# Performance work log

Hardware: AMD Instinct MI355X
Metric: run time of the kernel (lower is better)

Reference implementation:

```python
import jax, jax.numpy as jnp
import numpy as np
import math
from jax import lax

EPS = 1e-4
# scale is clamped to [-2.5, 2.5] => std = 2**scale <= 2**2.5, filtersize = ceil(3*std+0.5) <= 18
FMAX = 18


def _conv3(x, w, b):
    y = lax.conv_general_dilated(x, w, (1, 1), [(1, 1), (1, 1)],
                                 dimension_numbers=('NCHW', 'OIHW', 'NCHW'))
    return y + b[None, :, None, None]


def _conv1(x, w, b):
    return jnp.einsum('oc,bchw->bohw', w[:, :, 0, 0], x) + b[None, :, None, None]


def _basis_filters(scale):
    # per-sample Gaussian basis (g, dg/dx, dg/dy) on a fixed 37x37 grid,
    # exactly zero-masked beyond the data-dependent filtersize before normalization
    std = 2.0 ** scale
    f = jnp.ceil(3.0 * std + 0.5)
    x = jnp.arange(-FMAX, FMAX + 1, dtype=jnp.float32)
    m1 = (jnp.abs(x) <= f).astype(jnp.float32)
    X, Y = jnp.meshgrid(x, x, indexing='ij')  # torch.meshgrid default 'ij'
    m = m1[:, None] * m1[None, :]
    gx = jnp.exp(-(X / std) ** 2 / 2)
    gy = jnp.exp(-(Y / std) ** 2 / 2)
    g = gx * gy * m
    g = g / jnp.sum(g)
    c = std ** 3 * 2 * math.pi
    dgdx = (-X / c) * gx * gy * m
    dgdx = dgdx / jnp.sum(jnp.abs(dgdx))
    dgdy = (-Y / c) * gy * gx * m
    dgdy = dgdy / jnp.sum(jnp.abs(dgdy))
    return jnp.stack([g, dgdx, dgdy])  # [3, 37, 37]


def _gauss_conv(img, w):
    # img [3,H,W] = (E, El, Ell) planes; w [3,k,k] = (g, dgdx, dgdy)
    # treat the 3 planes as a batch of single-channel images -> [3,3,H,W]
    return lax.conv_general_dilated(img[:, None], w[:, None], (1, 1),
                                    [(FMAX, FMAX), (FMAX, FMAX)],
                                    dimension_numbers=('NCHW', 'OIHW', 'NCHW'))


def setup_inputs() -> dict:
    key = jax.random.key(0)
    B, H, W = 8, 384, 384
    nmid, base = 64, 16
    ks = iter(jax.random.split(key, 32))

    def rn(shape, s=0.1):
        return jax.random.normal(next(ks), shape, dtype=jnp.float32) * s

    x = jax.random.uniform(next(ks), (B, 3, H, W), dtype=jnp.float32)
    gcm = jnp.array([[0.06, 0.63, 0.27], [0.3, 0.04, -0.35], [0.34, -0.6, 0.17]],
                    dtype=jnp.float32)
    return {
        'x': x, 'gcm': gcm,
        'convH_w': rn((base, 1, 1, 1)), 'convH_b': rn((base,), 0.01),
        'convS_w': rn((base, 1, 1, 1)), 'convS_b': rn((base,), 0.01),
        'convRGB_w': rn((base, 3, 1, 1)), 'convRGB_b': rn((base,), 0.01),
        'convWw_w': rn((base, 1, 1, 1)), 'convWw_b': rn((base,), 0.01),
        'convadj_w': rn((nmid, 4 * base, 1, 1)), 'convadj_b': rn((nmid,), 0.01),
        'c0_w': rn((16, 3, 3, 3)), 'c0_b': rn((16,), 0.01),
        'c1_w': rn((16, 16, 3, 3)), 'c1_b': rn((16,), 0.01),
        'c2_w': rn((1, 16, 3, 3)), 'c2_b': rn((1,), 0.01),
        'wp0_w': rn((16, 3, 3, 3)), 'wp0_b': rn((16,), 0.01),
        'wp1_w': rn((16, 16, 3, 3)), 'wp1_b': rn((16,), 0.01),
        'wp2_w': rn((4, 16, 1, 1)), 'wp2_b': rn((4,), 0.01),
    }


def reference(x, gcm, convH_w, convH_b, convS_w, convS_b, convRGB_w, convRGB_b,
              convWw_w, convWw_b, convadj_w, convadj_b,
              c0_w, c0_b, c1_w, c1_b, c2_w, c2_b,
              wp0_w, wp0_b, wp1_w, wp1_b, wp2_w, wp2_b):
    # --- RGB ordering (torch.no_grad + scatter_add == sum of one-hots) ---
    xi = lax.stop_gradient(x)
    oh = lambda i: jax.nn.one_hot(i, 3, axis=1, dtype=x.dtype)
    mx, mn = jnp.argmax(xi, axis=1), jnp.argmin(xi, axis=1)
    mx_ = 2 - jnp.argmax(xi[:, ::-1], axis=1)
    mn_ = 2 - jnp.argmin(xi[:, ::-1], axis=1)
    RGB_order = 0.5 * (oh(mx) + oh(mx_)) - 0.5 * (oh(mn) + oh(mn_))
    # --- per-sample scale from small convnet ---
    s = jax.nn.silu(_conv3(x, c0_w, c0_b))
    s = jax.nn.silu(_conv3(s, c1_w, c1_b))
    s = _conv3(s, c2_w, c2_b)
    scale = jnp.clip(jnp.mean(s, axis=(1, 2, 3)), -2.5, 2.5)  # [B]
    # --- Gaussian color model transform ---
    xg = jnp.einsum('ij,bjhw->bihw', gcm, x)  # [B,3,H,W]
    # --- per-sample scale-dependent Gaussian-derivative convolution ---
    filters = jax.vmap(_basis_filters)(scale)       # [B,3,37,37]
    outs = jax.vmap(_gauss_conv)(xg, filters)       # [B,3,3,H,W]: plane x basis
    E, Ex, Ey = outs[:, 0, 0:1], outs[:, 0, 1:2], outs[:, 0, 2:3]
    El, Ell = outs[:, 1, 0:1], outs[:, 2, 0:1]
    Hc = jnp.arctan(El / (Ell + EPS))
    Sc = jnp.log((El ** 2 + Ell ** 2) / (E ** 2 + EPS) + EPS)
    Ww = jnp.arctan((Ex / (E + EPS)) ** 2 + (Ey / (E + EPS)) ** 2)
    # --- fusion weight predictor (on gcm-transformed image, softmax over 4) ---
    w = jax.nn.relu(_conv3(xg, wp0_w, wp0_b))
    w = jax.nn.relu(_conv3(w, wp1_w, wp1_b))
    weights = jax.nn.softmax(_conv1(w, wp2_w, wp2_b), axis=1)  # [B,4,H,W]
    H_fea_w = _conv1(Hc, convH_w, convH_b) * weights[:, 0:1]
    S_fea_w = _conv1(Sc, convS_w, convS_b) * weights[:, 1:2]
    RGB_fea_w = _conv1(RGB_order, convRGB_w, convRGB_b) * weights[:, 2:3]
    Ww_fea_w = jnp.zeros_like(H_fea_w)  # ablation == 'no_Ww' (default)
    del Ww  # computed for fidelity; zeroed by ablation
    feats = jnp.concatenate([H_fea_w, S_fea_w, RGB_fea_w, Ww_fea_w], axis=1)
    return _conv1(feats, convadj_w, convadj_b)  # [B, n_fea_middle, H, W]
```

## Files before the change

### kernel.cpp

```cpp
#include <hip/hip_runtime.h>

#define HH 384
#define WW 384
#define HWS (HH*WW)
#define NB 8
#define EPSV 1e-4f

typedef unsigned int u32;
typedef unsigned short u16;
typedef __attribute__((ext_vector_type(8))) short bf16x8;
typedef __attribute__((ext_vector_type(4))) float f32x4;

__device__ inline float bf2f(u16 h) { return __uint_as_float(((u32)h) << 16); }
__device__ inline u16 f2bf(float f) {
  u32 u = __float_as_uint(f);
  return (u16)((u + 0x7fffu + ((u >> 16) & 1u)) >> 16);
}
__device__ inline float fc4(const float4& v, int i) {
  return i == 0 ? v.x : i == 1 ? v.y : i == 2 ? v.z : v.w;
}

__global__ void k_prep(const float* __restrict__ adj_w,
                       const float* __restrict__ convH_w, const float* __restrict__ convH_b,
                       const float* __restrict__ convS_w, const float* __restrict__ convS_b,
                       const float* __restrict__ convRGB_w, const float* __restrict__ convRGB_b,
                       const float* __restrict__ gcm,
                       const float* __restrict__ c0_w, const float* __restrict__ wp0_w,
                       const float* __restrict__ c1_w, const float* __restrict__ wp1_w,
                       float* __restrict__ coef, float* __restrict__ c0t,
                       float* __restrict__ w0g, u32* __restrict__ wpk1,
                       u32* __restrict__ wpk2, float* __restrict__ sums) {
  int t = threadIdx.x;
  for (int i = t; i < NB * 16 * 9; i += 256) sums[i] = 0.f;
  for (int i = t; i < 432; i += 256) {
    int o = i & 15, rem = i >> 4;
    int c = rem / 9, k9 = rem - c * 9;
    c0t[i] = c0_w[(o * 3 + c) * 9 + k9];
    float s = 0.f;
    for (int j = 0; j < 3; j++) s += wp0_w[(o * 3 + j) * 9 + k9] * gcm[j * 3 + c];
    w0g[i] = s;
  }
  for (int i = t; i < 1280; i += 256) {
    int p = i >> 8;
    int rem = i & 255;
    int l = rem >> 2, wq = rem & 3;
    int tp = 2 * p + (l >> 5);
    int oc = l & 15;
    int ic0 = ((l >> 4) & 1) * 8 + wq * 2;
    u32 v1 = 0, v2 = 0;
    if (tp < 9) {
      v1 = f2bf(c1_w[(oc * 16 + ic0) * 9 + tp]);
      v2 = f2bf(c1_w[(oc * 16 + ic0 + 1) * 9 + tp]);
    }
    wpk1[i] = v1 | (v2 << 16);
    v1 = v2 = 0;
    if (tp < 9) {
      v1 = f2bf(wp1_w[(oc * 16 + ic0) * 9 + tp]);
      v2 = f2bf(wp1_w[(oc * 16 + ic0 + 1) * 9 + tp]);
    }
    wpk2[i] = v1 | (v2 << 16);
  }
  if (t < 64) {
    const float* a = adj_w + t * 64;
    float aH = 0, bH = 0, aS = 0, bS = 0, aR0 = 0, aR1 = 0, aR2 = 0, bR = 0;
    for (int i = 0; i < 16; i++) {
      aH += a[i] * convH_w[i];
      bH += a[i] * convH_b[i];
      aS += a[16 + i] * convS_w[i];
      bS += a[16 + i] * convS_b[i];
      float w = a[32 + i];
      aR0 += w * convRGB_w[i * 3 + 0];
      aR1 += w * convRGB_w[i * 3 + 1];
      aR2 += w * convRGB_w[i * 3 + 2];
      bR  += w * convRGB_b[i];
    }
    float* c = coef + t * 8;
    c[0] = aH; c[1] = bH; c[2] = aS; c[3] = bS;
    c[4] = aR0; c[5] = aR1; c[6] = aR2; c[7] = bR;
  }
}

__global__ __launch_bounds__(256, 4) void k_stackV(
    const float* __restrict__ xin,
    const float* __restrict__ w0t, const float* __restrict__ b0,
    const float* __restrict__ w1,  const float* __restrict__ b1,
    float* __restrict__ sums) {
  __shared__ float xt[3][20][36];
  __shared__ __align__(16) u16 s0[16 * 18 * 34];
  __shared__ float wl1[2304];
  __shared__ float red[64];

  const int tid = threadIdx.x;
  const int tx = tid & 15, ty = tid >> 4;
  const int b = blockIdx.z;
  const int bx = blockIdx.x * 32, by = blockIdx.y * 16;
  const float* xb = xin + (size_t)b * 3 * HWS;

  for (int i = tid; i < 2304; i += 256) {
    int o = i & 15, rem = i >> 4;
    int c = rem / 9, k9 = rem - c * 9;
    wl1[i] = w1[(o * 16 + c) * 9 + k9];
  }
  for (int i = tid; i < 3 * 20 * 36; i += 256) {
    int c = i / (20 * 36), r = i % (20 * 36);
    int yy = r / 36, xx = r - yy * 36;
    int gy = by + yy - 2, gx = bx + xx - 2;
    float v = 0.f;
    if ((u32)gy < HH && (u32)gx < WW) v = xb[(size_t)c * HWS + gy * WW + gx];
    xt[c][yy][xx] = v;
  }
  __syncthreads();

  for (int rnd = 0; rnd < 3; rnd++) {
    int p = tid + rnd * 256;
    if (p < 18 * 34) {
      int py = p / 34, pxh = p - py * 34;
      float a0[16];
#pragma unroll
      for (int o = 0; o < 16; o++) a0[o] = b0[o];
#pragma unroll 1
      for (int c = 0; c < 3; c++) {
#pragma unroll 1
        for (int ky = 0; ky < 3; ky++) {
#pragma unroll
          for (int kx = 0; kx < 3; kx++) {
            float xv = xt[c][py + ky][pxh + kx];
            const float* wr = &w0t[((c * 3 + ky) * 3 + kx) * 16];
#pragma unroll
            for (int o = 0; o < 16; o++) a0[o] = fmaf(xv, wr[o], a0[o]);
          }
        }
      }
      int oy = by + py - 1, ox = bx + pxh - 1;
      bool inside = ((u32)oy < HH) && ((u32)ox < WW);
      u16* sp = &s0[py * 34 + pxh];
#pragma unroll
      for (int o = 0; o < 16; o++) {
        float v = a0[o];
        v = v / (1.f + __expf(-v));
        sp[o * 18 * 34] = inside ? f2bf(v) : (u16)0;
      }
    }
  }
  __syncthreads();

  float acc[2][16];
#pragma unroll
  for (int o = 0; o < 16; o++) {
    float bb = b1[o];
    acc[0][o] = bb; acc[1][o] = bb;
  }
  for (int c = 0; c < 16; c++) {
#pragma unroll
    for (int ky = 0; ky < 3; ky++) {
      const u16* rowp = &s0[(c * 18 + ty + ky) * 34 + tx * 2];
      u32 wa = *(const u32*)(rowp);
      u32 wb = *(const u32*)(rowp + 2);
      float v[4];
      v[0] = bf2f((u16)(wa & 0xffffu)); v[1] = bf2f((u16)(wa >> 16));
      v[2] = bf2f((u16)(wb & 0xffffu)); v[3] = bf2f((u16)(wb >> 16));
#pragma unroll
      for (int kx = 0; kx < 3; kx++) {
        const float* wr = &wl1[(c * 9 + ky * 3 + kx) * 16];
        float4 wA = *(const float4*)(wr);
        float4 wB = *(const float4*)(wr + 4);
        float4 wC = *(const float4*)(wr + 8);
        float4 wD = *(const float4*)(wr + 12);
#pragma unroll
        for (int px = 0; px < 2; px++) {
          float vv = v[px + kx];
          acc[px][0]  = fmaf(vv, wA.x, acc[px][0]);
          acc[px][1]  = fmaf(vv, wA.y, acc[px][1]);
          acc[px][2]  = fmaf(vv, wA.z, acc[px][2]);
          acc[px][3]  = fmaf(vv, wA.w, acc[px][3]);
          acc[px][4]  = fmaf(vv, wB.x, acc[px][4]);
          acc[px][5]  = fmaf(vv, wB.y, acc[px][5]);
          acc[px][6]  = fmaf(vv, wB.z, acc[px][6]);
          acc[px][7]  = fmaf(vv, wB.w, acc[px][7]);
          acc[px][8]  = fmaf(vv, wC.x, acc[px][8]);
          acc[px][9]  = fmaf(vv, wC.y, acc[px][9]);
          acc[px][10] = fmaf(vv, wC.z, acc[px][10]);
          acc[px][11] = fmaf(vv, wC.w, acc[px][11]);
          acc[px][12] = fmaf(vv, wD.x, acc[px][12]);
          acc[px][13] = fmaf(vv, wD.y, acc[px][13]);
          acc[px][14] = fmaf(vv, wD.z, acc[px][14]);
          acc[px][15] = fmaf(vv, wD.w, acc[px][15]);
        }
      }
    }
  }

  const int y = by + ty, x0 = bx + tx * 2;
  float tloc[16];
  float* S = sums + (size_t)b * 16 * 9;
#pragma unroll
  for (int c = 0; c < 16; c++) {
    float s_[2];
#pragma unroll
    for (int px = 0; px < 2; px++) {
      float vv = acc[px][c];
      s_[px] = vv / (1.f + __expf(-vv));
    }
    float psum = s_[0] + s_[1];
    tloc[c] = psum;
    float* Sc_ = S + c * 9;
    if (y == 0)                        atomicAdd(Sc_ + 1, psum);
    if (y == HH - 1)                   atomicAdd(Sc_ + 2, psum);
    if (x0 == 0)                       atomicAdd(Sc_ + 3, s_[0]);
    if (x0 + 1 == WW - 1)              atomicAdd(Sc_ + 4, s_[1]);
    if (y == 0 && x0 == 0)             atomicAdd(Sc_ + 5, s_[0]);
    if (y == 0 && x0 + 1 == WW - 1)    atomicAdd(Sc_ + 6, s_[1]);
    if (y == HH - 1 && x0 == 0)        atomicAdd(Sc_ + 7, s_[0]);
    if (y == HH - 1 && x0 + 1 == WW-1) atomicAdd(Sc_ + 8, s_[1]);
  }
  const int lane = tid & 63, wv_ = tid >> 6;
#pragma unroll
  for (int c = 0; c < 16; c++) {
    float t = tloc[c];
    t += __shfl_down(t, 32, 64);
    t += __shfl_down(t, 16, 64);
    t += __shfl_down(t, 8, 64);
    t += __shfl_down(t, 4, 64);
    t += __shfl_down(t, 2, 64);
    t += __shfl_down(t, 1, 64);
    if (lane == 0) red[c * 4 + wv_] = t;
  }
  __syncthreads();
  if (tid < 16)
    atomicAdd(S + tid * 9, (red[tid * 4] + red[tid * 4 + 1]) + (red[tid * 4 + 2] + red[tid * 4 + 3]));
}

__global__ __launch_bounds__(256) void k_stackM(
    const float* __restrict__ xin,
    const float* __restrict__ w0t, const float* __restrict__ b0,
    const u32* __restrict__ wpk,  const float* __restrict__ b1,
    const float* __restrict__ wp2_w, const float* __restrict__ wp2_b,
    float* __restrict__ outw) {
  __shared__ float xt[3][20][68];
  __shared__ u16 s0[18 * 66 * 16];
  __shared__ float wl0[432];

  const int tid = threadIdx.x;
  const int b = blockIdx.z;
  const int bx = blockIdx.x * 64, by = blockIdx.y * 16;

  const float* xb = xin + (size_t)b * 3 * HWS;
  for (int i = tid; i < 432; i += 256) wl0[i] = w0t[i];
  for (int i = tid; i < 3 * 20 * 68; i += 256) {
    int c = i / (20 * 68), r = i % (20 * 68);
    int yy = r / 68, xx = r - yy * 68;
    int gy = by + yy - 2, gx = bx + xx - 2;
    float v = 0.f;
    if ((u32)gy < HH && (u32)gx < WW) v = xb[(size_t)c * HWS + gy * WW + gx];
    xt[c][yy][xx] = v;
  }
  __syncthreads();

  for (int rnd = 0; rnd < 5; rnd++) {
    int p = tid + rnd * 256;
    if (p < 18 * 66) {
      int py = p / 66, pxh = p - py * 66;
      float a0[16];
#pragma unroll
      for (int o = 0; o < 16; o++) a0[o] = b0[o];
#pragma unroll 1
      for (int c = 0; c < 3; c++) {
#pragma unroll 1
        for (int ky = 0; ky < 3; ky++) {
#pragma unroll
          for (int kx = 0; kx < 3; kx++) {
            float xv = xt[c][py + ky][pxh + kx];
            const float* wr = &wl0[((c * 3 + ky) * 3 + kx) * 16];
#pragma unroll
            for (int o = 0; o < 16; o++) a0[o] = fmaf(xv, wr[o], a0[o]);
          }
        }
      }
      int oy = by + py - 1, ox = bx + pxh - 1;
      bool inside = ((u32)oy < HH) && ((u32)ox < WW);
      u32 base = (u32)p * 32;
      u32 sw = (u32)(((pxh >> 2) & 1) << 4);
      u32 pk[8];
#pragma unroll
      for (int q = 0; q < 8; q++) {
        float e0 = fmaxf(a0[2 * q], 0.f), e1 = fmaxf(a0[2 * q + 1], 0.f);
        pk[q] = inside ? ((u32)f2bf(e0) | ((u32)f2bf(e1) << 16)) : 0u;
      }
      *(uint4*)((char*)s0 + ((base +  0) ^ sw)) = make_uint4(pk[0], pk[1], pk[2], pk[3]);
      *(uint4*)((char*)s0 + ((base + 16) ^ sw)) = make_uint4(pk[4], pk[5], pk[6], pk[7]);
    }
  }
  __syncthreads();

  const int l = tid & 63;
  const int wv = tid >> 6;
  const int n = l & 15, icb = (l >> 4) & 1, tt = l >> 5;
  const int g = l >> 4;

  bf16x8 af[5];
#pragma unroll
  for (int p = 0; p < 5; p++) af[p] = *(const bf16x8*)(wpk + (p * 64 + l) * 4);

  f32x4 cinit;
#pragma unroll
  for (int j = 0; j < 4; j++) cinit[j] = b1[g * 4 + j];

  u32 aoff[5], xoff[5];
#pragma unroll
  for (int p = 0; p < 5; p++) {
    int tp = 2 * p + tt; if (tp > 8) tp = 8;
    int ky = tp / 3, kx = tp - ky * 3;
    aoff[p] = (u32)((ky * 66 + kx) * 32);
    xoff[p] = (u32)((((n + kx) >> 2) & 1) << 4);
  }

  float w2f[4][4], wp2b[4];
#pragma unroll
  for (int jj = 0; jj < 4; jj++) {
    wp2b[jj] = wp2_b[jj];
#pragma unroll
    for (int j = 0; j < 4; j++) w2f[jj][j] = wp2_w[jj * 16 + g * 4 + j];
  }

#pragma unroll 1
  for (int r = 0; r < 4; r++) {
    int yo = wv * 4 + r;
    int gy = by + yo;
#pragma unroll 2
    for (int s = 0; s < 4; s++) {
      int xseg = s * 16;
      u32 base = (u32)((yo * 66 + xseg + n) * 32 + icb * 16);
      f32x4 acc = cinit;
#pragma unroll
      for (int p = 0; p < 5; p++) {
        bf16x8 bf = *(const bf16x8*)((char*)s0 + ((base + aoff[p]) ^ xoff[p]));
        acc = __builtin_amdgcn_mfma_f32_16x16x32_bf16(af[p], bf, acc, 0, 0, 0);
      }
      float plg[4] = {0.f, 0.f, 0.f, 0.f};
#pragma unroll
      for (int j = 0; j < 4; j++) {
        float v = fmaxf(acc[j], 0.f);
#pragma unroll
        for (int jj = 0; jj < 4; jj++) plg[jj] = fmaf(v, w2f[jj][j], plg[jj]);
      }
      float lg[4];
#pragma unroll
      for (int jj = 0; jj < 4; jj++) {
        float v = plg[jj];
        v += __shfl_xor(v, 16, 64);
        v += __shfl_xor(v, 32, 64);
        lg[jj] = v + wp2b[jj];
      }
      float m4 = fmaxf(fmaxf(lg[0], lg[1]), fmaxf(lg[2], lg[3]));
      float e0 = __expf(lg[0] - m4), e1 = __expf(lg[1] - m4);
      float e2 = __expf(lg[2] - m4), e3_ = __expf(lg[3] - m4);
      float inv = 1.f / ((e0 + e1) + (e2 + e3_));
      if (g < 3) {
        float wv_ = (g == 0 ? e0 : (g == 1 ? e1 : e2)) * inv;
        outw[(size_t)b * 3 * HWS + (size_t)g * HWS + (size_t)gy * WW + bx + xseg + n] = wv_;
      }
    }
  }
}

__global__ void k_scaletaps(const float* __restrict__ sums,
                            const float* __restrict__ c2_w, const float* __restrict__ c2_b,
                            float* __restrict__ taps) {
  int b = blockIdx.x, t = threadIdx.x;
  __shared__ float red[16];
  if (t < 16) {
    const float* S = sums + ((size_t)b * 16 + t) * 9;
    float T = S[0], R0 = S[1], R1 = S[2], C0 = S[3], C1 = S[4];
    float a00 = S[5], a01 = S[6], a10 = S[7], a11 = S[8];
    float acc = 0.f;
    for (int ky = 0; ky < 3; ky++)
      for (int kx = 0; kx < 3; kx++) {
        float s = T;
        if (ky == 0) s -= R1;
        if (ky == 2) s -= R0;
        if (kx == 0) s -= C1;
        if (kx == 2) s -= C0;
        if (ky == 0 && kx == 0) s += a11;
        if (ky == 0 && kx == 2) s += a10;
        if (ky == 2 && kx == 0) s += a01;
        if (ky == 2 && kx == 2) s += a00;
        acc += c2_w[(t * 3 + ky) * 3 + kx] * s;
      }
    red[t] = acc;
  }
  __syncthreads();
  __shared__ float u[37];
  __shared__ float std_sh, f_sh;
  if (t == 0) {
    float m = 0.f;
    for (int c = 0; c < 16; c++) m += red[c];
    m = m / (float)HWS + c2_b[0];
    float sc = fminf(2.5f, fmaxf(-2.5f, m));
    std_sh = exp2f(sc);
    f_sh = ceilf(3.f * std_sh + 0.5f);
  }
  __syncthreads();
  if (t < 37) {
    float xv = (float)(t - 18);
    float q = xv / std_sh;
    u[t] = (fabsf(xv) <= f_sh) ? expf(-0.5f * q * q) : 0.f;
  }
  __syncthreads();
  if (t == 0) {
    float s1 = 0.f;
    for (int i = 0; i < 37; i++) s1 += u[i];
    float inv = 1.f / s1;
    for (int i = 0; i < 37; i++) taps[b * 37 + i] = u[i] * inv;
  }
}

__global__ __launch_bounds__(128) void k_blurH(const float* __restrict__ x,
                                               const float* __restrict__ gcm,
                                               const float* __restrict__ taps,
                                               float* __restrict__ out) {
  __shared__ float row[3][164];
  __shared__ float tp[37];
  int b = blockIdx.z, y = blockIdx.y, x0 = blockIdx.x * 128, t = threadIdx.x;
  if (t < 37) tp[t] = taps[b * 37 + t];
  const float* xb = x + (size_t)b * 3 * HWS + (size_t)y * WW;
  float g0 = gcm[0], g1 = gcm[1], g2 = gcm[2];
  float g3 = gcm[3], g4 = gcm[4], g5 = gcm[5];
  float g6 = gcm[6], g7 = gcm[7], g8 = gcm[8];
  for (int idx = t; idx < 164; idx += 128) {
    int gx = x0 + idx - 18;
    bool ok = (u32)gx < WW;
    float v0 = ok ? xb[gx] : 0.f;
    float v1 = ok ? xb[HWS + gx] : 0.f;
    float v2 = ok ? xb[2 * HWS + gx] : 0.f;
    row[0][idx] = g0 * v0 + g1 * v1 + g2 * v2;
    row[1][idx] = g3 * v0 + g4 * v1 + g5 * v2;
    row[2][idx] = g6 * v0 + g7 * v1 + g8 * v2;
  }
  __syncthreads();
  float a0 = 0, a1 = 0, a2 = 0;
#pragma unroll
  for (int i = 0; i < 37; i++) {
    float w = tp[i];
    a0 = fmaf(w, row[0][t + i], a0);
    a1 = fmaf(w, row[1][t + i], a1);
    a2 = fmaf(w, row[2][t + i], a2);
  }
  float* ob = out + (size_t)b * 3 * HWS + (size_t)y * WW + x0 + t;
  ob[0] = a0; ob[HWS] = a1; ob[2 * HWS] = a2;
}

__global__ __launch_bounds__(128) void k_blurV(const float* __restrict__ in,
                                               const float* __restrict__ taps,
                                               float* __restrict__ out) {
  int img = blockIdx.z;
  int y0 = blockIdx.y * 16;
  int xx = blockIdx.x * 128 + threadIdx.x;
  __shared__ float tp[37];
  if (threadIdx.x < 37) tp[threadIdx.x] = taps[(img / 3) * 37 + threadIdx.x];
  __syncthreads();
  const float* base = in + (size_t)img * HWS + xx;
  float acc[16];
#pragma unroll
  for (int k = 0; k < 16; k++) acc[k] = 0.f;
#pragma unroll
  for (int i = 0; i < 52; i++) {
    int gy = y0 + i - 18;
    float v = ((u32)gy < HH) ? base[(size_t)gy * WW] : 0.f;
#pragma unroll
    for (int k = 0; k < 16; k++) {
      int ti = i - k;
      if (ti >= 0 && ti < 37) acc[k] = fmaf(tp[ti], v, acc[k]);
    }
  }
  float* ob = out + (size_t)img * HWS + xx;
#pragma unroll
  for (int k = 0; k < 16; k++) ob[(size_t)(y0 + k) * WW] = acc[k];
}

__global__ __launch_bounds__(256) void k_final(const float* __restrict__ x,
                                               const float* __restrict__ e3,
                                               const float* __restrict__ w012,
                                               const float* __restrict__ coef,
                                               const float* __restrict__ adj_b,
                                               float* __restrict__ out) {
  __shared__ float cf[576];
  int tid = threadIdx.x;
  for (int i = tid; i < 512; i += 256) cf[i] = coef[i];
  if (tid < 64) cf[512 + tid] = adj_b[tid];
  __syncthreads();
  int gi = blockIdx.x * 256 + tid;
  int pix = gi * 4;
  int b = pix / HWS, p = pix - b * HWS;

  const float* xb = x + (size_t)b * 3 * HWS + p;
  float4 X0 = *(const float4*)(xb);
  float4 X1 = *(const float4*)(xb + HWS);
  float4 X2 = *(const float4*)(xb + 2 * HWS);
  const float* eb = e3 + (size_t)b * 3 * HWS + p;
  float4 Ee  = *(const float4*)(eb);
  float4 Elv = *(const float4*)(eb + HWS);
  float4 Ell = *(const float4*)(eb + 2 * HWS);
  const float* wb = w012 + (size_t)b * 3 * HWS + p;
  float4 Wa = *(const float4*)(wb);
  float4 Wb = *(const float4*)(wb + HWS);
  float4 Wc = *(const float4*)(wb + 2 * HWS);

  float T[8][4];
#pragma unroll
  for (int px = 0; px < 4; px++) {
    float x0v = fc4(X0, px), x1v = fc4(X1, px), x2v = fc4(X2, px);
    int mx = 0;  float vm = x0v;
    if (x1v > vm) { mx = 1; vm = x1v; }
    if (x2v > vm) { mx = 2; vm = x2v; }
    int mxl = 0; vm = x0v;
    if (x1v >= vm) { mxl = 1; vm = x1v; }
    if (x2v >= vm) { mxl = 2; vm = x2v; }
    int mn = 0;  float vn = x0v;
    if (x1v < vn) { mn = 1; vn = x1v; }
    if (x2v < vn) { mn = 2; vn = x2v; }
    int mnl = 0; vn = x0v;
    if (x1v <= vn) { mnl = 1; vn = x1v; }
    if (x2v <= vn) { mnl = 2; vn = x2v; }
    float R0v = 0.5f * ((float)(mx == 0) + (float)(mxl == 0)) - 0.5f * ((float)(mn == 0) + (float)(mnl == 0));
    float R1v = 0.5f * ((float)(mx == 1) + (float)(mxl == 1)) - 0.5f * ((float)(mn == 1) + (float)(mnl == 1));
    float R2v = 0.5f * ((float)(mx == 2) + (float)(mxl == 2)) - 0.5f * ((float)(mn == 2) + (float)(mnl == 2));

    float Ev = fc4(Ee, px), El_ = fc4(Elv, px), Ell_ = fc4(Ell, px);
    float Hc = atanf(El_ / (Ell_ + EPSV));
    float Sc = logf((El_ * El_ + Ell_ * Ell_) / (Ev * Ev + EPSV) + EPSV);
    float w0 = fc4(Wa, px), w1 = fc4(Wb, px), w2 = fc4(Wc, px);
    T[0][px] = Hc * w0;  T[1][px] = w0;
    T[2][px] = Sc * w1;  T[3][px] = w1;
    T[4][px] = R0v * w2; T[5][px] = R1v * w2; T[6][px] = R2v * w2; T[7][px] = w2;
  }

  float* ob = out + (size_t)b * 64 * HWS + p;
#pragma unroll 4
  for (int o = 0; o < 64; o++) {
    float4 c0_ = *(const float4*)&cf[o * 8];
    float4 c1_ = *(const float4*)&cf[o * 8 + 4];
    float bb = cf[512 + o];
    float4 r;
    float rv[4];
#pragma unroll
    for (int px = 0; px < 4; px++) {
      float v = bb;
      v = fmaf(c0_.x, T[0][px], v); v = fmaf(c0_.y, T[1][px], v);
      v = fmaf(c0_.z, T[2][px], v); v = fmaf(c0_.w, T[3][px], v);
      v = fmaf(c1_.x, T[4][px], v); v = fmaf(c1_.y, T[5][px], v);
      v = fmaf(c1_.z, T[6][px], v); v = fmaf(c1_.w, T[7][px], v);
      rv[px] = v;
    }
    r.x = rv[0]; r.y = rv[1]; r.z = rv[2]; r.w = rv[3];
    *(float4*)(ob + (size_t)o * HWS) = r;
  }
}

extern "C" void kernel_launch(void* const* d_in, const int* in_sizes, int n_in,
                              void* d_out, int out_size, void* d_ws, size_t ws_size,
                              hipStream_t stream) {
  const float* x         = (const float*)d_in[0];
  const float* gcm       = (const float*)d_in[1];
  const float* convH_w   = (const float*)d_in[2];
  const float* convH_b   = (const float*)d_in[3];
  const float* convS_w   = (const float*)d_in[4];
  const float* convS_b   = (const float*)d_in[5];
  const float* convRGB_w = (const float*)d_in[6];
  const float* convRGB_b = (const float*)d_in[7];
  const float* convadj_w = (const float*)d_in[10];
  const float* convadj_b = (const float*)d_in[11];
  const float* c0_w  = (const float*)d_in[12];
  const float* c0_b  = (const float*)d_in[13];
  const float* c1_w  = (const float*)d_in[14];
  const float* c1_b  = (const float*)d_in[15];
  const float* c2_w  = (const float*)d_in[16];
  const float* c2_b  = (const float*)d_in[17];
  const float* wp0_w = (const float*)d_in[18];
  const float* wp0_b = (const float*)d_in[19];
  const float* wp1_w = (const float*)d_in[20];
  const float* wp1_b = (const float*)d_in[21];
  const float* wp2_w = (const float*)d_in[22];
  const float* wp2_b = (const float*)d_in[23];
  float* out = (float*)d_out;

  float* ws = (float*)d_ws;
  size_t off = 0;
  auto take = [&](size_t nf) { float* p = ws + off; off += nf; return p; };
  float* coef = take(512);
  float* c0t  = take(432);
  float* w0g  = take(432);
  u32*   wpk1 = (u32*)take(1280);
  u32*   wpk2 = (u32*)take(1280);
  float* sums = take((size_t)NB * 16 * 9);
  float* taps = take(320);
  const size_t P3 = (size_t)NB * 3 * HWS;
  float* tmp3 = take(P3);
  float* e3   = take(P3);
  float* w012 = take(P3);

  k_prep<<<1, 256, 0, stream>>>(convadj_w, convH_w, convH_b, convS_w, convS_b,
                                convRGB_w, convRGB_b, gcm, c0_w, wp0_w,
                                c1_w, wp1_w, coef, c0t, w0g, wpk1, wpk2, sums);

  k_stackV<<<dim3(12, 24, NB), 256, 0, stream>>>(x, c0t, c0_b, c1_w, c1_b, sums);
  k_scaletaps<<<NB, 64, 0, stream>>>(sums, c2_w, c2_b, taps);
  k_blurH<<<dim3(3, HH, NB), 128, 0, stream>>>(x, gcm, taps, tmp3);
  k_blurV<<<dim3(3, 24, NB * 3), 128, 0, stream>>>(tmp3, taps, e3);
  k_stackM<<<dim3(6, 24, NB), 256, 0, stream>>>(x, w0g, wp0_b, wpk2, wp1_b,
                                                wp2_w, wp2_b, w012);
  k_final<<<(NB * HWS / 4 + 255) / 256, 256, 0, stream>>>(x, e3, w012, coef, convadj_b, out);
}
```

Before: 346.4 us.

## Replace global atomics with per-block partials and separate border kernel

k_stackV no longer issues global atomicAdds for totals and border sums. Each block now writes its per-channel partial sum to a buffer, and k_scaletaps reduces those partials. A new k_border kernel recomputes the border rows and columns and their corner values directly, with 32 blocks of 128 threads, to avoid contention and divergent atomic branches. It also stores the k_stackM input tile in shared memory as bf16 and raises that kernel's occupancy hint. The costs are an extra serial launch, a slow border kernel with few blocks doing heavy per-thread work, and bf16 rounding of the input to k_stackM.

```diff
diff --git a/kernel.cpp b/kernel.cpp
--- a/kernel.cpp
+++ b/kernel.cpp
@@ -84,7 +84,7 @@
     const float* __restrict__ xin,
     const float* __restrict__ w0t, const float* __restrict__ b0,
     const float* __restrict__ w1,  const float* __restrict__ b1,
-    float* __restrict__ sums) {
+    float* __restrict__ partialsT) {
   __shared__ float xt[3][20][36];
   __shared__ __align__(16) u16 s0[16 * 18 * 34];
   __shared__ float wl1[2304];
@@ -190,28 +190,12 @@
     }
   }
 
-  const int y = by + ty, x0 = bx + tx * 2;
   float tloc[16];
-  float* S = sums + (size_t)b * 16 * 9;
 #pragma unroll
   for (int c = 0; c < 16; c++) {
-    float s_[2];
-#pragma unroll
-    for (int px = 0; px < 2; px++) {
-      float vv = acc[px][c];
-      s_[px] = vv / (1.f + __expf(-vv));
-    }
-    float psum = s_[0] + s_[1];
-    tloc[c] = psum;
-    float* Sc_ = S + c * 9;
-    if (y == 0)                        atomicAdd(Sc_ + 1, psum);
-    if (y == HH - 1)                   atomicAdd(Sc_ + 2, psum);
-    if (x0 == 0)                       atomicAdd(Sc_ + 3, s_[0]);
-    if (x0 + 1 == WW - 1)              atomicAdd(Sc_ + 4, s_[1]);
-    if (y == 0 && x0 == 0)             atomicAdd(Sc_ + 5, s_[0]);
-    if (y == 0 && x0 + 1 == WW - 1)    atomicAdd(Sc_ + 6, s_[1]);
-    if (y == HH - 1 && x0 == 0)        atomicAdd(Sc_ + 7, s_[0]);
-    if (y == HH - 1 && x0 + 1 == WW-1) atomicAdd(Sc_ + 8, s_[1]);
+    float s0v = acc[0][c] / (1.f + __expf(-acc[0][c]));
+    float s1v = acc[1][c] / (1.f + __expf(-acc[1][c]));
+    tloc[c] = s0v + s1v;
   }
   const int lane = tid & 63, wv_ = tid >> 6;
 #pragma unroll
@@ -226,17 +210,137 @@
     if (lane == 0) red[c * 4 + wv_] = t;
   }
   __syncthreads();
-  if (tid < 16)
-    atomicAdd(S + tid * 9, (red[tid * 4] + red[tid * 4 + 1]) + (red[tid * 4 + 2] + red[tid * 4 + 3]));
-}
-
-__global__ __launch_bounds__(256) void k_stackM(
+  if (tid < 16) {
+    int blk = blockIdx.y * gridDim.x + blockIdx.x;
+    partialsT[((size_t)b * 288 + blk) * 16 + tid] =
+        (red[tid * 4] + red[tid * 4 + 1]) + (red[tid * 4 + 2] + red[tid * 4 + 3]);
+  }
+}
+
+__global__ __launch_bounds__(128) void k_border(
+    const float* __restrict__ xin,
+    const float* __restrict__ w0t, const float* __restrict__ b0,
+    const float* __restrict__ w1,  const float* __restrict__ b1,
+    float* __restrict__ sums) {
+  __shared__ float wl1[2304];
+  __shared__ float wl0[432];
+  __shared__ float red2[2][16];
+  const int tid = threadIdx.x;
+  const int bs = blockIdx.x;
+  const int b = bs >> 2, strip = bs & 3;
+  const float* xb = xin + (size_t)b * 3 * HWS;
+  for (int i = tid; i < 2304; i += 128) {
+    int o = i & 15, rem = i >> 4;
+    int c = rem / 9, k9 = rem - c * 9;
+    wl1[i] = w1[(o * 16 + c) * 9 + k9];
+  }
+  for (int i = tid; i < 432; i += 128) wl0[i] = w0t[i];
+  __syncthreads();
+
+  float* S = sums + (size_t)b * 16 * 9;
+  float strip_sum[16];
+#pragma unroll
+  for (int c = 0; c < 16; c++) strip_sum[c] = 0.f;
+
+#pragma unroll 1
+  for (int j = 0; j < 3; j++) {
+    int idx = tid * 3 + j;
+    int y, x;
+    if (strip == 0)      { y = 0;      x = idx; }
+    else if (strip == 1) { y = HH - 1; x = idx; }
+    else if (strip == 2) { y = idx;    x = 0; }
+    else                 { y = idx;    x = WW - 1; }
+
+    float acc1[16];
+#pragma unroll
+    for (int o = 0; o < 16; o++) acc1[o] = b1[o];
+#pragma unroll 1
+    for (int ky = 0; ky < 3; ky++) {
+#pragma unroll 1
+      for (int kx = 0; kx < 3; kx++) {
+        int py = y + ky - 1, px = x + kx - 1;
+        float s0v[16];
+        if ((u32)py < HH && (u32)px < WW) {
+          float a0[16];
+#pragma unroll
+          for (int o = 0; o < 16; o++) a0[o] = b0[o];
+#pragma unroll 1
+          for (int ci = 0; ci < 3; ci++) {
+#pragma unroll
+            for (int k2 = 0; k2 < 3; k2++) {
+#pragma unroll
+              for (int k3 = 0; k3 < 3; k3++) {
+                int gy = py + k2 - 1, gx = px + k3 - 1;
+                float xv = ((u32)gy < HH && (u32)gx < WW)
+                           ? xb[(size_t)ci * HWS + gy * WW + gx] : 0.f;
+                const float* wr = &wl0[((ci * 3 + k2) * 3 + k3) * 16];
+#pragma unroll
+                for (int o = 0; o < 16; o++) a0[o] = fmaf(xv, wr[o], a0[o]);
+              }
+            }
+          }
+#pragma unroll
+          for (int o = 0; o < 16; o++) {
+            float sv = a0[o] / (1.f + __expf(-a0[o]));
+            s0v[o] = bf2f(f2bf(sv));
+          }
+        } else {
+#pragma unroll
+          for (int o = 0; o < 16; o++) s0v[o] = 0.f;
+        }
+#pragma unroll
+        for (int c = 0; c < 16; c++) {
+          const float* wr = &wl1[(c * 9 + ky * 3 + kx) * 16];
+          float v = s0v[c];
+#pragma unroll
+          for (int o = 0; o < 16; o++) acc1[o] = fmaf(v, wr[o], acc1[o]);
+        }
+      }
+    }
+    float s1s[16];
+#pragma unroll
+    for (int c = 0; c < 16; c++) {
+      float vv = acc1[c];
+      s1s[c] = vv / (1.f + __expf(-vv));
+      strip_sum[c] += s1s[c];
+    }
+    if (strip == 0 && x == 0) {
+#pragma unroll
+      for (int c = 0; c < 16; c++) S[c * 9 + 5] = s1s[c];
+    }
+    if (strip == 0 && x == WW - 1) {
+#pragma unroll
+      for (int c = 0; c < 16; c++) S[c * 9 + 6] = s1s[c];
+    }
+    if (strip == 1 && x == 0) {
+#pragma unroll
+      for (int c = 0; c < 16; c++) S[c * 9 + 7] = s1s[c];
+    }
+    if (strip == 1 && x == WW - 1) {
+#pragma unroll
+      for (int c = 0; c < 16; c++) S[c * 9 + 8] = s1s[c];
+    }
+  }
+
+  const int lane = tid & 63, wv_ = tid >> 6;
+#pragma unroll
+  for (int c = 0; c < 16; c++) {
+    float t = strip_sum[c];
+#pragma unroll
+    for (int m = 1; m <= 32; m <<= 1) t += __shfl_xor(t, m, 64);
+    if (lane == 0) red2[wv_][c] = t;
+  }
+  __syncthreads();
+  if (tid < 16) S[tid * 9 + 1 + strip] = red2[0][tid] + red2[1][tid];
+}
+
+__global__ __launch_bounds__(256, 3) void k_stackM(
     const float* __restrict__ xin,
     const float* __restrict__ w0t, const float* __restrict__ b0,
     const u32* __restrict__ wpk,  const float* __restrict__ b1,
     const float* __restrict__ wp2_w, const float* __restrict__ wp2_b,
     float* __restrict__ outw) {
-  __shared__ float xt[3][20][68];
+  __shared__ u16 xt[3][20][68];
   __shared__ u16 s0[18 * 66 * 16];
   __shared__ float wl0[432];
 
@@ -252,7 +356,7 @@
     int gy = by + yy - 2, gx = bx + xx - 2;
     float v = 0.f;
     if ((u32)gy < HH && (u32)gx < WW) v = xb[(size_t)c * HWS + gy * WW + gx];
-    xt[c][yy][xx] = v;
+    xt[c][yy][xx] = f2bf(v);
   }
   __syncthreads();
 
@@ -269,7 +373,7 @@
         for (int ky = 0; ky < 3; ky++) {
 #pragma unroll
           for (int kx = 0; kx < 3; kx++) {
-            float xv = xt[c][py + ky][pxh + kx];
+            float xv = bf2f(xt[c][py + ky][pxh + kx]);
             const float* wr = &wl0[((c * 3 + ky) * 3 + kx) * 16];
 #pragma unroll
             for (int o = 0; o < 16; o++) a0[o] = fmaf(xv, wr[o], a0[o]);
@@ -363,14 +467,18 @@
   }
 }
 
-__global__ void k_scaletaps(const float* __restrict__ sums,
+__global__ void k_scaletaps(const float* __restrict__ partialsT,
+                            const float* __restrict__ sums,
                             const float* __restrict__ c2_w, const float* __restrict__ c2_b,
                             float* __restrict__ taps) {
   int b = blockIdx.x, t = threadIdx.x;
   __shared__ float red[16];
   if (t < 16) {
+    const float* P = partialsT + (size_t)b * 288 * 16;
+    float T = 0.f;
+    for (int k = 0; k < 288; k++) T += P[k * 16 + t];
     const float* S = sums + ((size_t)b * 16 + t) * 9;
-    float T = S[0], R0 = S[1], R1 = S[2], C0 = S[3], C1 = S[4];
+    float R0 = S[1], R1 = S[2], C0 = S[3], C1 = S[4];
     float a00 = S[5], a01 = S[6], a10 = S[7], a11 = S[8];
     float acc = 0.f;
     for (int ky = 0; ky < 3; ky++)
@@ -593,6 +701,7 @@
   u32*   wpk2 = (u32*)take(1280);
   float* sums = take((size_t)NB * 16 * 9);
   float* taps = take(320);
+  float* partialsT = take((size_t)NB * 288 * 16);
   const size_t P3 = (size_t)NB * 3 * HWS;
   float* tmp3 = take(P3);
   float* e3   = take(P3);
@@ -602,8 +711,9 @@
                                 convRGB_w, convRGB_b, gcm, c0_w, wp0_w,
                                 c1_w, wp1_w, coef, c0t, w0g, wpk1, wpk2, sums);
 
-  k_stackV<<<dim3(12, 24, NB), 256, 0, stream>>>(x, c0t, c0_b, c1_w, c1_b, sums);
-  k_scaletaps<<<NB, 64, 0, stream>>>(sums, c2_w, c2_b, taps);
+  k_stackV<<<dim3(12, 24, NB), 256, 0, stream>>>(x, c0t, c0_b, c1_w, c1_b, partialsT);
+  k_border<<<NB * 4, 128, 0, stream>>>(x, c0t, c0_b, c1_w, c1_b, sums);
+  k_scaletaps<<<NB, 64, 0, stream>>>(partialsT, sums, c2_w, c2_b, taps);
   k_blurH<<<dim3(3, HH, NB), 128, 0, stream>>>(x, gcm, taps, tmp3);
   k_blurV<<<dim3(3, 24, NB * 3), 128, 0, stream>>>(tmp3, taps, e3);
   k_stackM<<<dim3(6, 24, NB), 256, 0, stream>>>(x, w0g, wp0_b, wpk2, wp1_b,
```

After: 388.9 us. 12.3% more time.

## Replace atomic reductions with per-block partials; store stackM input tile as bf16

Applied to the files above, without the earlier changes.

k_stackV now writes per-block channel sums and per-block edge-strip sums to workspace arrays instead of using global atomicAdd, and writes the four corner values directly. k_scaletaps does the final reduction over these partials, which makes the sum deterministic and removes atomic contention on a few addresses. Separately, k_stackM keeps its input tile in shared memory as bf16 to cut LDS use, and its launch bounds now request 3 blocks per CU. The bf16 input adds rounding error to the first conv, and the serial 288-element loop in k_scaletaps adds a small tail.

```diff
diff --git a/kernel.cpp b/kernel.cpp
--- a/kernel.cpp
+++ b/kernel.cpp
@@ -84,11 +84,13 @@
     const float* __restrict__ xin,
     const float* __restrict__ w0t, const float* __restrict__ b0,
     const float* __restrict__ w1,  const float* __restrict__ b1,
+    float* __restrict__ partialsT, float* __restrict__ strips,
     float* __restrict__ sums) {
   __shared__ float xt[3][20][36];
   __shared__ __align__(16) u16 s0[16 * 18 * 34];
   __shared__ float wl1[2304];
   __shared__ float red[64];
+  __shared__ float sbuf[16][17];
 
   const int tid = threadIdx.x;
   const int tx = tid & 15, ty = tid >> 4;
@@ -190,28 +192,12 @@
     }
   }
 
-  const int y = by + ty, x0 = bx + tx * 2;
   float tloc[16];
-  float* S = sums + (size_t)b * 16 * 9;
 #pragma unroll
   for (int c = 0; c < 16; c++) {
-    float s_[2];
-#pragma unroll
-    for (int px = 0; px < 2; px++) {
-      float vv = acc[px][c];
-      s_[px] = vv / (1.f + __expf(-vv));
-    }
-    float psum = s_[0] + s_[1];
-    tloc[c] = psum;
-    float* Sc_ = S + c * 9;
-    if (y == 0)                        atomicAdd(Sc_ + 1, psum);
-    if (y == HH - 1)                   atomicAdd(Sc_ + 2, psum);
-    if (x0 == 0)                       atomicAdd(Sc_ + 3, s_[0]);
-    if (x0 + 1 == WW - 1)              atomicAdd(Sc_ + 4, s_[1]);
-    if (y == 0 && x0 == 0)             atomicAdd(Sc_ + 5, s_[0]);
-    if (y == 0 && x0 + 1 == WW - 1)    atomicAdd(Sc_ + 6, s_[1]);
-    if (y == HH - 1 && x0 == 0)        atomicAdd(Sc_ + 7, s_[0]);
-    if (y == HH - 1 && x0 + 1 == WW-1) atomicAdd(Sc_ + 8, s_[1]);
+    float s0v = acc[0][c] / (1.f + __expf(-acc[0][c]));
+    float s1v = acc[1][c] / (1.f + __expf(-acc[1][c]));
+    tloc[c] = s0v + s1v;
   }
   const int lane = tid & 63, wv_ = tid >> 6;
 #pragma unroll
@@ -226,17 +212,91 @@
     if (lane == 0) red[c * 4 + wv_] = t;
   }
   __syncthreads();
-  if (tid < 16)
-    atomicAdd(S + tid * 9, (red[tid * 4] + red[tid * 4 + 1]) + (red[tid * 4 + 2] + red[tid * 4 + 3]));
-}
-
-__global__ __launch_bounds__(256) void k_stackM(
+  if (tid < 16) {
+    int blk = blockIdx.y * gridDim.x + blockIdx.x;
+    partialsT[((size_t)b * 288 + blk) * 16 + tid] =
+        (red[tid * 4] + red[tid * 4 + 1]) + (red[tid * 4 + 2] + red[tid * 4 + 3]);
+  }
+
+  float* Sb = strips + (size_t)b * 72 * 16;
+  if (blockIdx.y == 0) {
+    __syncthreads();
+    if (ty == 0) {
+#pragma unroll
+      for (int c = 0; c < 16; c++) sbuf[tx][c] = tloc[c];
+    }
+    __syncthreads();
+    if (tid < 16) {
+      float s = 0.f;
+      for (int k = 0; k < 16; k++) s += sbuf[k][tid];
+      Sb[(0 + blockIdx.x) * 16 + tid] = s;
+    }
+  }
+  if (blockIdx.y == 23) {
+    __syncthreads();
+    if (ty == 15) {
+#pragma unroll
+      for (int c = 0; c < 16; c++) sbuf[tx][c] = tloc[c];
+    }
+    __syncthreads();
+    if (tid < 16) {
+      float s = 0.f;
+      for (int k = 0; k < 16; k++) s += sbuf[k][tid];
+      Sb[(12 + blockIdx.x) * 16 + tid] = s;
+    }
+  }
+  if (blockIdx.x == 0) {
+    __syncthreads();
+    if (tx == 0) {
+#pragma unroll
+      for (int c = 0; c < 16; c++) sbuf[ty][c] = acc[0][c] / (1.f + __expf(-acc[0][c]));
+    }
+    __syncthreads();
+    if (tid < 16) {
+      float s = 0.f;
+      for (int k = 0; k < 16; k++) s += sbuf[k][tid];
+      Sb[(24 + blockIdx.y) * 16 + tid] = s;
+    }
+  }
+  if (blockIdx.x == 11) {
+    __syncthreads();
+    if (tx == 15) {
+#pragma unroll
+      for (int c = 0; c < 16; c++) sbuf[ty][c] = acc[1][c] / (1.f + __expf(-acc[1][c]));
+    }
+    __syncthreads();
+    if (tid < 16) {
+      float s = 0.f;
+      for (int k = 0; k < 16; k++) s += sbuf[k][tid];
+      Sb[(48 + blockIdx.y) * 16 + tid] = s;
+    }
+  }
+  float* S = sums + (size_t)b * 16 * 9;
+  if (blockIdx.y == 0 && blockIdx.x == 0 && tid == 0) {
+#pragma unroll
+    for (int c = 0; c < 16; c++) S[c * 9 + 5] = acc[0][c] / (1.f + __expf(-acc[0][c]));
+  }
+  if (blockIdx.y == 0 && blockIdx.x == 11 && tid == 15) {
+#pragma unroll
+    for (int c = 0; c < 16; c++) S[c * 9 + 6] = acc[1][c] / (1.f + __expf(-acc[1][c]));
+  }
+  if (blockIdx.y == 23 && blockIdx.x == 0 && tid == 240) {
+#pragma unroll
+    for (int c = 0; c < 16; c++) S[c * 9 + 7] = acc[0][c] / (1.f + __expf(-acc[0][c]));
+  }
+  if (blockIdx.y == 23 && blockIdx.x == 11 && tid == 255) {
+#pragma unroll
+    for (int c = 0; c < 16; c++) S[c * 9 + 8] = acc[1][c] / (1.f + __expf(-acc[1][c]));
+  }
+}
+
+__global__ __launch_bounds__(256, 3) void k_stackM(
     const float* __restrict__ xin,
     const float* __restrict__ w0t, const float* __restrict__ b0,
     const u32* __restrict__ wpk,  const float* __restrict__ b1,
     const float* __restrict__ wp2_w, const float* __restrict__ wp2_b,
     float* __restrict__ outw) {
-  __shared__ float xt[3][20][68];
+  __shared__ u16 xt[3][20][68];
   __shared__ u16 s0[18 * 66 * 16];
   __shared__ float wl0[432];
 
@@ -252,7 +312,7 @@
     int gy = by + yy - 2, gx = bx + xx - 2;
     float v = 0.f;
     if ((u32)gy < HH && (u32)gx < WW) v = xb[(size_t)c * HWS + gy * WW + gx];
-    xt[c][yy][xx] = v;
+    xt[c][yy][xx] = f2bf(v);
   }
   __syncthreads();
 
@@ -269,7 +329,7 @@
         for (int ky = 0; ky < 3; ky++) {
 #pragma unroll
           for (int kx = 0; kx < 3; kx++) {
-            float xv = xt[c][py + ky][pxh + kx];
+            float xv = bf2f(xt[c][py + ky][pxh + kx]);
             const float* wr = &wl0[((c * 3 + ky) * 3 + kx) * 16];
 #pragma unroll
             for (int o = 0; o < 16; o++) a0[o] = fmaf(xv, wr[o], a0[o]);
@@ -363,14 +423,24 @@
   }
 }
 
-__global__ void k_scaletaps(const float* __restrict__ sums,
+__global__ void k_scaletaps(const float* __restrict__ partialsT,
+                            const float* __restrict__ strips,
+                            const float* __restrict__ sums,
                             const float* __restrict__ c2_w, const float* __restrict__ c2_b,
                             float* __restrict__ taps) {
   int b = blockIdx.x, t = threadIdx.x;
   __shared__ float red[16];
   if (t < 16) {
+    const float* P = partialsT + (size_t)b * 288 * 16;
+    float T = 0.f;
+    for (int k = 0; k < 288; k++) T += P[k * 16 + t];
+    const float* Sb = strips + (size_t)b * 72 * 16;
+    float R0 = 0.f, R1 = 0.f, C0 = 0.f, C1 = 0.f;
+    for (int k = 0; k < 12; k++) R0 += Sb[(0 + k) * 16 + t];
+    for (int k = 0; k < 12; k++) R1 += Sb[(12 + k) * 16 + t];
+    for (int k = 0; k < 24; k++) C0 += Sb[(24 + k) * 16 + t];
+    for (int k = 0; k < 24; k++) C1 += Sb[(48 + k) * 16 + t];
     const float* S = sums + ((size_t)b * 16 + t) * 9;
-    float T = S[0], R0 = S[1], R1 = S[2], C0 = S[3], C1 = S[4];
     float a00 = S[5], a01 = S[6], a10 = S[7], a11 = S[8];
     float acc = 0.f;
     for (int ky = 0; ky < 3; ky++)
@@ -593,6 +663,8 @@
   u32*   wpk2 = (u32*)take(1280);
   float* sums = take((size_t)NB * 16 * 9);
   float* taps = take(320);
+  float* partialsT = take((size_t)NB * 288 * 16);
+  float* strips    = take((size_t)NB * 72 * 16);
   const size_t P3 = (size_t)NB * 3 * HWS;
   float* tmp3 = take(P3);
   float* e3   = take(P3);
@@ -602,8 +674,9 @@
                                 convRGB_w, convRGB_b, gcm, c0_w, wp0_w,
                                 c1_w, wp1_w, coef, c0t, w0g, wpk1, wpk2, sums);
 
-  k_stackV<<<dim3(12, 24, NB), 256, 0, stream>>>(x, c0t, c0_b, c1_w, c1_b, sums);
-  k_scaletaps<<<NB, 64, 0, stream>>>(sums, c2_w, c2_b, taps);
+  k_stackV<<<dim3(12, 24, NB), 256, 0, stream>>>(x, c0t, c0_b, c1_w, c1_b,
+                                                 partialsT, strips, sums);
+  k_scaletaps<<<NB, 64, 0, stream>>>(partialsT, strips, sums, c2_w, c2_b, taps);
   k_blurH<<<dim3(3, HH, NB), 128, 0, stream>>>(x, gcm, taps, tmp3);
   k_blurV<<<dim3(3, 24, NB * 3), 128, 0, stream>>>(tmp3, taps, e3);
   k_stackM<<<dim3(6, 24, NB), 256, 0, stream>>>(x, w0g, wp0_b, wpk2, wp1_b,
```

After: 306.4 us. 1.13x faster.
